# Performance work log

Measured on AMD Instinct MI355X. Metric: run time of the kernel, lower is better.

Reference implementation:

```python
import jax, jax.numpy as jnp
import numpy as np

D = 2048
H = 16
HD = 128
INNER = H * HD
EPS = 1e-6


def rmsnorm(x, w):
    var = jnp.mean(x * x, axis=-1, keepdims=True)
    return x * jax.lax.rsqrt(var + EPS) * w


def setup_inputs() -> dict:
    key = jax.random.key(0)
    ks = jax.random.split(key, 10)
    B, T, N_ws, T_corr = 2, 2048, 64, 512
    scale = 1.0 / np.sqrt(D)
    return {
        "hidden_states": jax.random.normal(ks[0], (B, T, D), jnp.float32),
        "workspace": jax.random.normal(ks[1], (B, N_ws, D), jnp.float32),
        "correction_tokens": jax.random.normal(ks[2], (B, T_corr, D), jnp.float32),
        "correction_mask": jax.random.randint(ks[3], (B, T_corr), 0, 2, jnp.int32),
        "ln_q_w": jnp.ones((D,), jnp.float32),
        "ln_kv_w": jnp.ones((D,), jnp.float32),
        "Wq": jax.random.normal(ks[4], (D, INNER), jnp.float32) * scale,
        "Wk": jax.random.normal(ks[5], (D, INNER), jnp.float32) * scale,
        "Wv": jax.random.normal(ks[6], (D, INNER), jnp.float32) * scale,
        "Wo": jax.random.normal(ks[7], (INNER, D), jnp.float32) * scale,
    }


def reference(hidden_states, workspace, correction_tokens, correction_mask,
              ln_q_w, ln_kv_w, Wq, Wk, Wv, Wo):
    B, T, _ = hidden_states.shape
    N_ws = workspace.shape[1]
    # kv context = [workspace ; correction_tokens]
    kv_context = jnp.concatenate([workspace, correction_tokens], axis=1)  # (B, N_kv, D)
    N_kv = kv_context.shape[1]
    ws_mask = jnp.ones((B, N_ws), hidden_states.dtype)
    kv_mask = jnp.concatenate([ws_mask, correction_mask.astype(hidden_states.dtype)], axis=1)  # (B, N_kv)

    h = rmsnorm(hidden_states, ln_q_w)
    kv = rmsnorm(kv_context, ln_kv_w)

    q = (h @ Wq).reshape(B, T, H, HD)        # (B,T,H,hd)
    k = (kv @ Wk).reshape(B, N_kv, H, HD)
    v = (kv @ Wv).reshape(B, N_kv, H, HD)

    scores = jnp.einsum("bthd,bshd->bhts", q, k) / np.sqrt(HD)  # (B,H,T,N_kv)
    mask = (kv_mask != 0)[:, None, None, :]                      # (B,1,1,N_kv)
    scores = jnp.where(mask, scores, -jnp.inf)
    attn = jax.nn.softmax(scores, axis=-1)
    attn = jnp.nan_to_num(attn, nan=0.0)
    # dropout is identity in eval mode
    out = jnp.einsum("bhts,bshd->bthd", attn, v).reshape(B, T, INNER)
    return out @ Wo
```

## Files before the change

kernel.cpp:

```cpp
#include <hip/hip_runtime.h>
#include <hip/hip_bf16.h>
#include <math.h>

typedef __bf16 bf16;
typedef __attribute__((ext_vector_type(8))) __bf16 bf16x8;
typedef __attribute__((ext_vector_type(4))) __bf16 bf16x4;
typedef __attribute__((ext_vector_type(4))) float f32x4;

#define D_DIM 2048
#define NKV   576

__device__ inline void gld_lds16(const void* g, void* l) {
    void* gg = const_cast<void*>(g);
    __builtin_amdgcn_global_load_lds(
        (__attribute__((address_space(1))) void*)gg,
        (__attribute__((address_space(3))) void*)l, 16, 0, 0);
}

__global__ __launch_bounds__(256) void prep(
    const float* __restrict__ hidden, const float* __restrict__ wsp,
    const float* __restrict__ corr, const float* __restrict__ lnq,
    const float* __restrict__ lnkv,
    const float* __restrict__ Wq, const float* __restrict__ Wk,
    const float* __restrict__ Wv, const float* __restrict__ Wo,
    bf16* __restrict__ hb, bf16* __restrict__ kvb,
    bf16* __restrict__ WqT, bf16* __restrict__ WkvT, bf16* __restrict__ WoT)
{
    __shared__ float tile[32][33];
    __shared__ float p[4];
    const int id = blockIdx.x, t = threadIdx.x;

    if (id < 16384) {
        const int wz = id >> 12, wy = (id >> 6) & 63, wx = id & 63;
        const float* in; bf16* out;
        switch (wz) {
            case 0:  in = Wq; out = WqT; break;
            case 1:  in = Wk; out = WkvT; break;
            case 2:  in = Wv; out = WkvT + 2048ull * 2048; break;
            default: in = Wo; out = WoT; break;
        }
        const int r0 = wy * 32, c0 = wx * 32;
        const int r = t >> 3, c = (t & 7) * 4;
        float4 v = *(const float4*)(in + (long)(r0 + r) * 2048 + c0 + c);
        tile[r][c] = v.x; tile[r][c + 1] = v.y;
        tile[r][c + 2] = v.z; tile[r][c + 3] = v.w;
        __syncthreads();
        bf16x4 o = { (bf16)tile[c][r], (bf16)tile[c + 1][r],
                     (bf16)tile[c + 2][r], (bf16)tile[c + 3][r] };
        *(bf16x4*)(out + (long)(c0 + r) * 2048 + r0 + c) = o;
        return;
    }

    const int rr0 = id - 16384;
    const float* xr; const float* w; bf16* yr;
    if (rr0 < 4096) {
        xr = hidden + (long)rr0 * D_DIM; w = lnq; yr = hb + (long)rr0 * D_DIM;
    } else if (rr0 < 4224) {
        const int rr = rr0 - 4096;
        xr = wsp + (long)rr * D_DIM; w = lnkv;
        yr = kvb + ((long)(rr >> 6) * NKV + (rr & 63)) * D_DIM;
    } else {
        const int rr = rr0 - 4224;
        xr = corr + (long)rr * D_DIM; w = lnkv;
        yr = kvb + ((long)(rr >> 9) * NKV + 64 + (rr & 511)) * D_DIM;
    }

    float4 v0 = *(const float4*)(xr + t * 4);
    float4 v1 = *(const float4*)(xr + 1024 + t * 4);
    float ss = v0.x * v0.x + v0.y * v0.y + v0.z * v0.z + v0.w * v0.w
             + v1.x * v1.x + v1.y * v1.y + v1.z * v1.z + v1.w * v1.w;
#pragma unroll
    for (int off = 32; off; off >>= 1) ss += __shfl_xor(ss, off);
    if ((t & 63) == 0) p[t >> 6] = ss;
    __syncthreads();
    const float rs = rsqrtf((p[0] + p[1] + p[2] + p[3]) * (1.0f / 2048.0f) + 1e-6f);

    float4 w0 = *(const float4*)(w + t * 4);
    float4 w1 = *(const float4*)(w + 1024 + t * 4);
    bf16x4 o0 = { (bf16)(v0.x * rs * w0.x), (bf16)(v0.y * rs * w0.y),
                  (bf16)(v0.z * rs * w0.z), (bf16)(v0.w * rs * w0.w) };
    bf16x4 o1 = { (bf16)(v1.x * rs * w1.x), (bf16)(v1.y * rs * w1.y),
                  (bf16)(v1.z * rs * w1.z), (bf16)(v1.w * rs * w1.w) };
    *(bf16x4*)(yr + t * 4) = o0;
    *(bf16x4*)(yr + 1024 + t * 4) = o1;
}

__global__ __launch_bounds__(256) void proj_all(
    const bf16* __restrict__ hb, const bf16* __restrict__ kvb,
    const bf16* __restrict__ WqT, const bf16* __restrict__ WkvT,
    bf16* __restrict__ qb, bf16* __restrict__ kb, bf16* __restrict__ vtb)
{
    __shared__ __align__(16) bf16 smem[128 * 132];
    bf16* As = smem;
    bf16* Bs = smem + 128 * 64;

    int id = blockIdx.x;
    const bf16 *A, *B; int m0, n0; bool isQ;
    if (id < 512) {
        isQ = true; A = hb; B = WqT;
        m0 = (id >> 4) * 128; n0 = (id & 15) * 128;
    } else {
        id -= 512;
        isQ = false; A = kvb; B = WkvT;
        m0 = (id >> 5) * 128; n0 = (id & 31) * 128;
    }
    const int tid = threadIdx.x, lane = tid & 63;
    const int wm = ((tid >> 6) >> 1) * 64, wn = ((tid >> 6) & 1) * 64;
    const int fr = lane & 15, fg = lane >> 4;

    f32x4 acc[4][4] = {};

    for (int k0 = 0; k0 < 2048; k0 += 64) {
#pragma unroll
        for (int p = 0; p < 4; ++p) {
            const int c = p * 256 + tid;
            const int r = c >> 3, cl = (c & 7) ^ (r & 7);
            gld_lds16(A + (long)(m0 + r) * 2048 + k0 + cl * 8, As + c * 8);
            gld_lds16(B + (long)(n0 + r) * 2048 + k0 + cl * 8, Bs + c * 8);
        }
        __syncthreads();
#pragma unroll
        for (int s = 0; s < 2; ++s) {
            const int sl = ((s << 2) + fg) ^ (fr & 7);
            bf16x8 af[4], bg[4];
#pragma unroll
            for (int i = 0; i < 4; ++i)
                af[i] = *(const bf16x8*)(As + (((wm + i * 16 + fr) << 3) + sl) * 8);
#pragma unroll
            for (int j = 0; j < 4; ++j)
                bg[j] = *(const bf16x8*)(Bs + (((wn + j * 16 + fr) << 3) + sl) * 8);
#pragma unroll
            for (int i = 0; i < 4; ++i)
#pragma unroll
                for (int j = 0; j < 4; ++j)
                    acc[i][j] = __builtin_amdgcn_mfma_f32_16x16x32_bf16(
                        af[i], bg[j], acc[i][j], 0, 0, 0);
        }
        __syncthreads();
    }

    const int er = fg * 4;
    if (isQ || n0 < 2048) {
        bf16* C = isQ ? qb : kb;
        const int ldc = 2048;
#pragma unroll
        for (int i = 0; i < 4; ++i)
#pragma unroll
            for (int j = 0; j < 4; ++j) {
                const int n = n0 + wn + j * 16 + fr;
#pragma unroll
                for (int r = 0; r < 4; ++r)
                    C[(long)(m0 + wm + i * 16 + er + r) * ldc + n] = (bf16)acc[i][j][r];
            }
        return;
    }

    const int h = (n0 - 2048) >> 7;
#pragma unroll
    for (int i = 0; i < 4; ++i)
#pragma unroll
        for (int j = 0; j < 4; ++j) {
            const int nl = wn + j * 16 + fr;
#pragma unroll
            for (int r = 0; r < 4; ++r)
                smem[nl * 132 + (wm + i * 16 + er + r)] = (bf16)acc[i][j][r];
        }
    __syncthreads();
#pragma unroll
    for (int p = 0; p < 16; ++p) {
        const int e = p * 1024 + tid * 4;
        const int d = e >> 7, mloc = e & 127;
        bf16x4 val = *(const bf16x4*)(smem + d * 132 + mloc);
        const int mm = m0 + mloc;
        const int bb = mm >= NKV;
        const int s = mm - bb * NKV;
        *(bf16x4*)(vtb + ((long)((bb * 16 + h) * 128 + d)) * NKV + s) = val;
    }
}

__global__ __launch_bounds__(256) void gemm_final(
    const bf16* __restrict__ A, const bf16* __restrict__ B, float* __restrict__ C)
{
    __shared__ __align__(16) bf16 As[128 * 64];
    __shared__ __align__(16) bf16 Bs[128 * 64];

    const int m0 = blockIdx.y * 128, n0 = blockIdx.x * 128;
    const int tid = threadIdx.x, lane = tid & 63;
    const int wm = ((tid >> 6) >> 1) * 64, wn = ((tid >> 6) & 1) * 64;
    const int fr = lane & 15, fg = lane >> 4;

    f32x4 acc[4][4] = {};

    for (int k0 = 0; k0 < 2048; k0 += 64) {
#pragma unroll
        for (int p = 0; p < 4; ++p) {
            const int c = p * 256 + tid;
            const int r = c >> 3, cl = (c & 7) ^ (r & 7);
            gld_lds16(A + (long)(m0 + r) * 2048 + k0 + cl * 8, As + c * 8);
            gld_lds16(B + (long)(n0 + r) * 2048 + k0 + cl * 8, Bs + c * 8);
        }
        __syncthreads();
#pragma unroll
        for (int s = 0; s < 2; ++s) {
            const int sl = ((s << 2) + fg) ^ (fr & 7);
            bf16x8 af[4], bg[4];
#pragma unroll
            for (int i = 0; i < 4; ++i)
                af[i] = *(const bf16x8*)(As + (((wm + i * 16 + fr) << 3) + sl) * 8);
#pragma unroll
            for (int j = 0; j < 4; ++j)
                bg[j] = *(const bf16x8*)(Bs + (((wn + j * 16 + fr) << 3) + sl) * 8);
#pragma unroll
            for (int i = 0; i < 4; ++i)
#pragma unroll
                for (int j = 0; j < 4; ++j)
                    acc[i][j] = __builtin_amdgcn_mfma_f32_16x16x32_bf16(
                        af[i], bg[j], acc[i][j], 0, 0, 0);
        }
        __syncthreads();
    }

    const int er = fg * 4;
#pragma unroll
    for (int i = 0; i < 4; ++i)
#pragma unroll
        for (int j = 0; j < 4; ++j) {
            const int n = n0 + wn + j * 16 + fr;
#pragma unroll
            for (int r = 0; r < 4; ++r)
                C[(long)(m0 + wm + i * 16 + er + r) * 2048 + n] = acc[i][j][r];
        }
}

__global__ __launch_bounds__(256, 4) void flash_attn(
    const bf16* __restrict__ Q, const bf16* __restrict__ K,
    const bf16* __restrict__ VT, const int* __restrict__ cmask,
    bf16* __restrict__ O)
{
    __shared__ __align__(16) bf16 Ks[64 * 128];
    __shared__ __align__(16) bf16 VTs[128 * 64];

    const int qt = blockIdx.x, h = blockIdx.y, b = blockIdx.z;
    const int tid = threadIdx.x, lane = tid & 63, w = tid >> 6;
    const int fr = lane & 15, fg = lane >> 4;

    const bf16* qbase = Q + ((long)(b * 2048 + qt * 64)) * 2048 + h * 128;
    bf16x8 qf[4];
#pragma unroll
    for (int s = 0; s < 4; ++s)
        qf[s] = *(const bf16x8*)(qbase + (long)(w * 16 + fr) * 2048 + s * 32 + fg * 8);

    float m_r[4], l_r[4];
    f32x4 acc_o[8];
#pragma unroll
    for (int r = 0; r < 4; ++r) { m_r[r] = -3.0e38f; l_r[r] = 0.f; }
#pragma unroll
    for (int j = 0; j < 8; ++j) acc_o[j] = (f32x4){0.f, 0.f, 0.f, 0.f};

    const float scale2 = 0.12752792330124195f;
    const bf16* kbase = K + (long)b * NKV * 2048 + h * 128;
    const bf16* vbase = VT + ((long)(b * 16 + h)) * 128 * NKV;

    for (int kc = 0; kc < 9; ++kc) {
        const int kv0 = kc * 64;
#pragma unroll
        for (int p = 0; p < 4; ++p) {
            const int c = p * 256 + tid;
            const int r = c >> 4, cs = c & 15, cl = cs ^ (r & 15);
            gld_lds16(kbase + (long)(kv0 + r) * 2048 + cl * 8, Ks + c * 8);
        }
#pragma unroll
        for (int p = 0; p < 4; ++p) {
            const int c = p * 256 + tid;
            const int r = c >> 3, cs = c & 7, cl = cs ^ (r & 7);
            gld_lds16(vbase + (long)r * NKV + kv0 + cl * 8, VTs + c * 8);
        }
        __syncthreads();

        f32x4 acc_s[4] = {};
#pragma unroll
        for (int s = 0; s < 4; ++s) {
#pragma unroll
            for (int j = 0; j < 4; ++j) {
                bf16x8 bg = *(const bf16x8*)(Ks +
                    ((j * 16 + fr) * 16 + ((s * 4 + fg) ^ fr)) * 8);
                acc_s[j] = __builtin_amdgcn_mfma_f32_16x16x32_bf16(qf[s], bg, acc_s[j], 0, 0, 0);
            }
        }

        float bias[4];
#pragma unroll
        for (int j = 0; j < 4; ++j) {
            const int kv = kv0 + j * 16 + fr;
            const bool valid = (kv < 64) || (cmask[b * 512 + kv - 64] != 0);
            bias[j] = valid ? 0.f : -1e30f;
        }
        float s_f[4][4];
        float mc[4] = {-3.0e38f, -3.0e38f, -3.0e38f, -3.0e38f};
#pragma unroll
        for (int j = 0; j < 4; ++j)
#pragma unroll
            for (int r = 0; r < 4; ++r) {
                float v = fmaf(acc_s[j][r], scale2, bias[j]);
                s_f[j][r] = v; mc[r] = fmaxf(mc[r], v);
            }
#pragma unroll
        for (int r = 0; r < 4; ++r) {
            mc[r] = fmaxf(mc[r], __shfl_xor(mc[r], 1));
            mc[r] = fmaxf(mc[r], __shfl_xor(mc[r], 2));
            mc[r] = fmaxf(mc[r], __shfl_xor(mc[r], 4));
            mc[r] = fmaxf(mc[r], __shfl_xor(mc[r], 8));
        }
        float alpha[4];
#pragma unroll
        for (int r = 0; r < 4; ++r) {
            const float mn = fmaxf(m_r[r], mc[r]);
            alpha[r] = __builtin_amdgcn_exp2f(m_r[r] - mn);
            m_r[r] = mn;
        }
        float rs[4] = {0.f, 0.f, 0.f, 0.f};
#pragma unroll
        for (int j = 0; j < 4; ++j)
#pragma unroll
            for (int r = 0; r < 4; ++r) {
                const float pv = __builtin_amdgcn_exp2f(s_f[j][r] - m_r[r]);
                s_f[j][r] = pv; rs[r] += pv;
            }
#pragma unroll
        for (int r = 0; r < 4; ++r) {
            rs[r] += __shfl_xor(rs[r], 1);
            rs[r] += __shfl_xor(rs[r], 2);
            rs[r] += __shfl_xor(rs[r], 4);
            rs[r] += __shfl_xor(rs[r], 8);
            l_r[r] = l_r[r] * alpha[r] + rs[r];
        }
#pragma unroll
        for (int j = 0; j < 8; ++j)
#pragma unroll
            for (int r = 0; r < 4; ++r) acc_o[j][r] *= alpha[r];

        __syncthreads();

        bf16* Ps = Ks;
#pragma unroll
        for (int j = 0; j < 4; ++j)
#pragma unroll
            for (int r = 0; r < 4; ++r)
                Ps[(w * 16 + fg * 4 + r) * 72 + j * 16 + fr] = (bf16)s_f[j][r];

#pragma unroll
        for (int s2 = 0; s2 < 2; ++s2) {
            bf16x8 af = *(const bf16x8*)(Ps + (w * 16 + fr) * 72 + s2 * 32 + fg * 8);
#pragma unroll
            for (int jd = 0; jd < 8; ++jd) {
                bf16x8 bg = *(const bf16x8*)(VTs +
                    ((jd * 16 + fr) * 8 + ((s2 * 4 + fg) ^ (fr & 7))) * 8);
                acc_o[jd] = __builtin_amdgcn_mfma_f32_16x16x32_bf16(af, bg, acc_o[jd], 0, 0, 0);
            }
        }
        __syncthreads();
    }

    bf16* obase = O + ((long)(b * 2048 + qt * 64)) * 2048 + h * 128;
#pragma unroll
    for (int r = 0; r < 4; ++r) {
        const float inv = 1.0f / l_r[r];
        const int row = w * 16 + fg * 4 + r;
#pragma unroll
        for (int jd = 0; jd < 8; ++jd)
            obase[(long)row * 2048 + jd * 16 + fr] = (bf16)(acc_o[jd][r] * inv);
    }
}

extern "C" void kernel_launch(void* const* d_in, const int* in_sizes, int n_in,
                              void* d_out, int out_size, void* d_ws, size_t ws_size,
                              hipStream_t stream)
{
    const float* hidden = (const float*)d_in[0];
    const float* wsp    = (const float*)d_in[1];
    const float* corr   = (const float*)d_in[2];
    const int*   cmask  = (const int*)d_in[3];
    const float* lnq    = (const float*)d_in[4];
    const float* lnkv   = (const float*)d_in[5];
    const float* Wq     = (const float*)d_in[6];
    const float* Wk     = (const float*)d_in[7];
    const float* Wv     = (const float*)d_in[8];
    const float* Wo     = (const float*)d_in[9];
    float* out = (float*)d_out;

    char* ws = (char*)d_ws;
    size_t off = 0;
    auto alloc = [&](size_t sz) { void* p = ws + off; off += (sz + 255) & ~(size_t)255; return p; };

    bf16* WqT   = (bf16*)alloc(2048ull * 2048 * 2);
    bf16* WkvT  = (bf16*)alloc(4096ull * 2048 * 2);
    bf16* WoT   = (bf16*)alloc(2048ull * 2048 * 2);
    bf16* hb    = (bf16*)alloc(4096ull * 2048 * 2);
    bf16* kvb   = (bf16*)alloc(1152ull * 2048 * 2);
    bf16* qb    = (bf16*)alloc(4096ull * 2048 * 2);
    bf16* kb    = (bf16*)alloc(1152ull * 2048 * 2);
    bf16* vtb   = (bf16*)alloc(4096ull * NKV * 2);
    bf16* aob   = (bf16*)alloc(4096ull * 2048 * 2);

    prep<<<21632, 256, 0, stream>>>(hidden, wsp, corr, lnq, lnkv,
                                    Wq, Wk, Wv, Wo, hb, kvb, WqT, WkvT, WoT);
    proj_all<<<800, 256, 0, stream>>>(hb, kvb, WqT, WkvT, qb, kb, vtb);
    flash_attn<<<dim3(32, 16, 2), 256, 0, stream>>>(qb, kb, vtb, cmask, aob);
    gemm_final<<<dim3(16, 32), 256, 0, stream>>>(aob, WoT, out);
}
```

Before: 325.0 us.

## Rewrite projection and output GEMMs as 8-wave 256-tile ping-pong pipelined kernels

Both the QKV projection and the output GEMM move from 128x128 single-buffered tiles with 4 waves to 512-thread blocks with 256-row tiles. They use double-buffered LDS (even/odd stages), async global-to-LDS loads interleaved with MFMA phases under fine-grained barriers and vmcnt waits, and s_setprio around MFMA bursts. Block IDs are remapped for L2 locality. The goal is to hide global load latency and raise arithmetic intensity, at the cost of more LDS and registers per block. The kv buffer is padded to 1280 rows so the final tile may read past the valid 1152 rows, and stores are guarded against those rows.

```diff
diff --git a/kernel.cpp b/kernel.cpp
--- a/kernel.cpp
+++ b/kernel.cpp
@@ -16,6 +16,9 @@
         (__attribute__((address_space(1))) void*)gg,
         (__attribute__((address_space(3))) void*)l, 16, 0, 0);
 }
+
+#define PH_BARRIER() do { __builtin_amdgcn_s_barrier(); asm volatile("" ::: "memory"); } while (0)
+#define VMCNT(n)     asm volatile("s_waitcnt vmcnt(" #n ")" ::: "memory")
 
 __global__ __launch_bounds__(256) void prep(
     const float* __restrict__ hidden, const float* __restrict__ wsp,
@@ -85,140 +88,251 @@
     *(bf16x4*)(yr + 1024 + t * 4) = o1;
 }
 
-__global__ __launch_bounds__(256) void proj_all(
+__global__ __launch_bounds__(512, 2) void proj_all(
     const bf16* __restrict__ hb, const bf16* __restrict__ kvb,
     const bf16* __restrict__ WqT, const bf16* __restrict__ WkvT,
     bf16* __restrict__ qb, bf16* __restrict__ kb, bf16* __restrict__ vtb)
 {
-    __shared__ __align__(16) bf16 smem[128 * 132];
-    bf16* As = smem;
-    bf16* Bs = smem + 128 * 64;
-
-    int id = blockIdx.x;
+    __shared__ __align__(16) bf16 smem[4][16384];
+    bf16* const EA = smem[0]; bf16* const EB = smem[1];
+    bf16* const OA = smem[2]; bf16* const OB = smem[3];
+
+    const int id0 = blockIdx.x;
+    const int id = (id0 & 7) * 26 + (id0 >> 3);
     const bf16 *A, *B; int m0, n0; bool isQ;
-    if (id < 512) {
-        isQ = true; A = hb; B = WqT;
-        m0 = (id >> 4) * 128; n0 = (id & 15) * 128;
+    if (id < 128) {
+        isQ = true;  A = hb;  B = WqT;
+        m0 = (id >> 3) * 256; n0 = (id & 7) * 256;
     } else {
-        id -= 512;
+        const int kd = id - 128;
         isQ = false; A = kvb; B = WkvT;
-        m0 = (id >> 5) * 128; n0 = (id & 31) * 128;
-    }
-    const int tid = threadIdx.x, lane = tid & 63;
-    const int wm = ((tid >> 6) >> 1) * 64, wn = ((tid >> 6) & 1) * 64;
+        m0 = (kd >> 4) * 256; n0 = (kd & 15) * 256;
+    }
+
+    const int tid = threadIdx.x, lane = tid & 63, w = tid >> 6;
+    const int wm = (w >> 2) * 128, wn = (w & 3) * 64;
     const int fr = lane & 15, fg = lane >> 4;
 
-    f32x4 acc[4][4] = {};
-
-    for (int k0 = 0; k0 < 2048; k0 += 64) {
-#pragma unroll
-        for (int p = 0; p < 4; ++p) {
-            const int c = p * 256 + tid;
+    f32x4 acc[8][4] = {};
+    bf16x8 af[4][2], bg[4][2];
+
+    auto stage = [&](const bf16* base, int row0, int k, bf16* dst) {
+#pragma unroll
+        for (int q = 0; q < 2; ++q) {
+            const int c = q * 512 + tid;
             const int r = c >> 3, cl = (c & 7) ^ (r & 7);
-            gld_lds16(A + (long)(m0 + r) * 2048 + k0 + cl * 8, As + c * 8);
-            gld_lds16(B + (long)(n0 + r) * 2048 + k0 + cl * 8, Bs + c * 8);
-        }
-        __syncthreads();
-#pragma unroll
-        for (int s = 0; s < 2; ++s) {
-            const int sl = ((s << 2) + fg) ^ (fr & 7);
-            bf16x8 af[4], bg[4];
+            gld_lds16(base + (long)(row0 + r) * 2048 + k + cl * 8, dst + c * 8);
+        }
+    };
+    auto load_af = [&](const bf16* t, int ib) {
+#pragma unroll
+        for (int i = 0; i < 4; ++i)
+#pragma unroll
+            for (int s = 0; s < 2; ++s) {
+                const int row = wm + (ib + i) * 16 + fr;
+                af[i][s] = *(const bf16x8*)(t + ((row << 3) + ((s * 4 + fg) ^ (fr & 7))) * 8);
+            }
+    };
+    auto load_bg = [&](const bf16* t, int jb) {
+#pragma unroll
+        for (int j = 0; j < 2; ++j)
+#pragma unroll
+            for (int s = 0; s < 2; ++s) {
+                const int row = wn + (jb + j) * 16 + fr;
+                bg[jb + j][s] = *(const bf16x8*)(t + ((row << 3) + ((s * 4 + fg) ^ (fr & 7))) * 8);
+            }
+    };
+    auto mfma16 = [&](int ib, int jb) {
+        __builtin_amdgcn_s_setprio(1);
+#pragma unroll
+        for (int s = 0; s < 2; ++s)
 #pragma unroll
             for (int i = 0; i < 4; ++i)
-                af[i] = *(const bf16x8*)(As + (((wm + i * 16 + fr) << 3) + sl) * 8);
-#pragma unroll
-            for (int j = 0; j < 4; ++j)
-                bg[j] = *(const bf16x8*)(Bs + (((wn + j * 16 + fr) << 3) + sl) * 8);
-#pragma unroll
-            for (int i = 0; i < 4; ++i)
-#pragma unroll
-                for (int j = 0; j < 4; ++j)
-                    acc[i][j] = __builtin_amdgcn_mfma_f32_16x16x32_bf16(
-                        af[i], bg[j], acc[i][j], 0, 0, 0);
-        }
-        __syncthreads();
-    }
+#pragma unroll
+                for (int j = 0; j < 2; ++j)
+                    acc[ib + i][jb + j] = __builtin_amdgcn_mfma_f32_16x16x32_bf16(
+                        af[i][s], bg[jb + j][s], acc[ib + i][jb + j], 0, 0, 0);
+        __builtin_amdgcn_s_setprio(0);
+    };
+
+    stage(A, m0,        0, EA); stage(A, m0 + 128,  0, EA + 8192);
+    stage(B, n0,        0, EB); stage(B, n0 + 128,  0, EB + 8192);
+    stage(B, n0,       64, OB); stage(B, n0 + 128, 64, OB + 8192);
+    VMCNT(4);
+    PH_BARRIER();
+
+    for (int it = 0; it < 16; ++it) {
+        const int kO  = (it * 128 +  64) & 2047;
+        const int kE2 = (it * 128 + 128) & 2047;
+        const int kO2 = (it * 128 + 192) & 2047;
+        load_af(EA, 0); load_bg(EB, 0);
+        stage(A, m0, kO, OA);
+        PH_BARRIER(); mfma16(0, 0); PH_BARRIER();
+        load_bg(EB, 2);
+        stage(A, m0 + 128, kO, OA + 8192);
+        PH_BARRIER(); mfma16(0, 2); PH_BARRIER();
+        load_af(EA, 4);
+        stage(B, n0, kE2, EB);
+        PH_BARRIER(); mfma16(4, 2); PH_BARRIER();
+        stage(B, n0 + 128, kE2, EB + 8192);
+        PH_BARRIER(); mfma16(4, 0); VMCNT(4); PH_BARRIER();
+        load_af(OA, 0); load_bg(OB, 0);
+        stage(A, m0, kE2, EA);
+        PH_BARRIER(); mfma16(0, 0); PH_BARRIER();
+        load_bg(OB, 2);
+        stage(A, m0 + 128, kE2, EA + 8192);
+        PH_BARRIER(); mfma16(0, 2); PH_BARRIER();
+        load_af(OA, 4);
+        stage(B, n0, kO2, OB);
+        PH_BARRIER(); mfma16(4, 2); PH_BARRIER();
+        stage(B, n0 + 128, kO2, OB + 8192);
+        PH_BARRIER(); mfma16(4, 0); VMCNT(4); PH_BARRIER();
+    }
+
+    VMCNT(0);
+    __syncthreads();
 
     const int er = fg * 4;
     if (isQ || n0 < 2048) {
         bf16* C = isQ ? qb : kb;
-        const int ldc = 2048;
-#pragma unroll
-        for (int i = 0; i < 4; ++i)
+        const int mlim = isQ ? 4096 : 1152;
+#pragma unroll
+        for (int i = 0; i < 8; ++i)
 #pragma unroll
             for (int j = 0; j < 4; ++j) {
                 const int n = n0 + wn + j * 16 + fr;
 #pragma unroll
-                for (int r = 0; r < 4; ++r)
-                    C[(long)(m0 + wm + i * 16 + er + r) * ldc + n] = (bf16)acc[i][j][r];
+                for (int r = 0; r < 4; ++r) {
+                    const int m = m0 + wm + i * 16 + er + r;
+                    if (m < mlim)
+                        C[(long)m * 2048 + n] = (bf16)acc[i][j][r];
+                }
             }
         return;
     }
 
-    const int h = (n0 - 2048) >> 7;
-#pragma unroll
-    for (int i = 0; i < 4; ++i)
-#pragma unroll
-        for (int j = 0; j < 4; ++j) {
-            const int nl = wn + j * 16 + fr;
-#pragma unroll
-            for (int r = 0; r < 4; ++r)
-                smem[nl * 132 + (wm + i * 16 + er + r)] = (bf16)acc[i][j][r];
-        }
+    bf16* T = &smem[0][0];
+#pragma unroll
+    for (int p = 0; p < 2; ++p) {
+        if (p) __syncthreads();
+        if ((wn >> 7) == p) {
+            const int nb = wn - p * 128;
+#pragma unroll
+            for (int i = 0; i < 8; ++i)
+#pragma unroll
+                for (int j = 0; j < 4; ++j) {
+                    const int nl = nb + j * 16 + fr;
+#pragma unroll
+                    for (int r = 0; r < 4; ++r)
+                        T[nl * 264 + wm + i * 16 + er + r] = (bf16)acc[i][j][r];
+                }
+        }
+        __syncthreads();
+        const int hh = (n0 - 2048 + p * 128) >> 7;
+        for (int e = tid; e < 128 * 64; e += 512) {
+            const int d = e >> 6, mg = (e & 63) * 4;
+            const int mm = m0 + mg;
+            if (mm < 1152) {
+                bf16x4 val = *(const bf16x4*)(T + d * 264 + mg);
+                const int bb = mm >= NKV;
+                const int s = mm - bb * NKV;
+                *(bf16x4*)(vtb + ((long)((bb * 16 + hh) * 128 + d)) * NKV + s) = val;
+            }
+        }
+    }
+}
+
+__global__ __launch_bounds__(512, 2) void gemm_final(
+    const bf16* __restrict__ Ag, const bf16* __restrict__ Bg, float* __restrict__ C)
+{
+    __shared__ __align__(16) bf16 smem[49152];
+    bf16* const EA = smem;           bf16* const EB = smem + 16384;
+    bf16* const OA = smem + 24576;   bf16* const OB = smem + 40960;
+
+    const int id0 = blockIdx.x;
+    const int id = (id0 & 7) * 32 + (id0 >> 3);
+    const int m0 = (id >> 4) * 256, n0 = (id & 15) * 128;
+
+    const int tid = threadIdx.x, lane = tid & 63, w = tid >> 6;
+    const int wm = (w >> 1) * 64, wn = (w & 1) * 64;
+    const int fr = lane & 15, fg = lane >> 4;
+
+    f32x4 acc[4][4] = {};
+    bf16x8 af[2][2], bg[4][2];
+
+    auto stage = [&](const bf16* base, int row0, int k, bf16* dst) {
+#pragma unroll
+        for (int q = 0; q < 2; ++q) {
+            const int c = q * 512 + tid;
+            const int r = c >> 3, cl = (c & 7) ^ (r & 7);
+            gld_lds16(base + (long)(row0 + r) * 2048 + k + cl * 8, dst + c * 8);
+        }
+    };
+    auto load_af = [&](const bf16* t, int ib) {
+#pragma unroll
+        for (int i = 0; i < 2; ++i)
+#pragma unroll
+            for (int s = 0; s < 2; ++s) {
+                const int row = wm + (ib + i) * 16 + fr;
+                af[i][s] = *(const bf16x8*)(t + ((row << 3) + ((s * 4 + fg) ^ (fr & 7))) * 8);
+            }
+    };
+    auto load_bg = [&](const bf16* t, int jb) {
+#pragma unroll
+        for (int j = 0; j < 2; ++j)
+#pragma unroll
+            for (int s = 0; s < 2; ++s) {
+                const int row = wn + (jb + j) * 16 + fr;
+                bg[jb + j][s] = *(const bf16x8*)(t + ((row << 3) + ((s * 4 + fg) ^ (fr & 7))) * 8);
+            }
+    };
+    auto mfma8 = [&](int ib, int jb) {
+        __builtin_amdgcn_s_setprio(1);
+#pragma unroll
+        for (int s = 0; s < 2; ++s)
+#pragma unroll
+            for (int i = 0; i < 2; ++i)
+#pragma unroll
+                for (int j = 0; j < 2; ++j)
+                    acc[ib + i][jb + j] = __builtin_amdgcn_mfma_f32_16x16x32_bf16(
+                        af[i][s], bg[jb + j][s], acc[ib + i][jb + j], 0, 0, 0);
+        __builtin_amdgcn_s_setprio(0);
+    };
+
+    stage(Ag, m0,       0, EA); stage(Ag, m0 + 128, 0, EA + 8192);
+    stage(Bg, n0,       0, EB);
+    stage(Bg, n0,      64, OB);
+    VMCNT(2);
+    PH_BARRIER();
+
+    for (int it = 0; it < 16; ++it) {
+        const int kO  = (it * 128 +  64) & 2047;
+        const int kE2 = (it * 128 + 128) & 2047;
+        const int kO2 = (it * 128 + 192) & 2047;
+        load_af(EA, 0); load_bg(EB, 0);
+        stage(Ag, m0, kO, OA);
+        PH_BARRIER(); mfma8(0, 0); PH_BARRIER();
+        load_bg(EB, 2);
+        stage(Ag, m0 + 128, kO, OA + 8192);
+        PH_BARRIER(); mfma8(0, 2); PH_BARRIER();
+        load_af(EA, 2);
+        stage(Bg, n0, kE2, EB);
+        PH_BARRIER(); mfma8(2, 2); PH_BARRIER();
+        stage(Ag, m0, kE2, EA);
+        PH_BARRIER(); mfma8(2, 0); VMCNT(4); PH_BARRIER();
+        load_af(OA, 0); load_bg(OB, 0);
+        stage(Ag, m0 + 128, kE2, EA + 8192);
+        PH_BARRIER(); mfma8(0, 0); PH_BARRIER();
+        load_bg(OB, 2);
+        PH_BARRIER(); mfma8(0, 2); PH_BARRIER();
+        load_af(OA, 2);
+        stage(Bg, n0, kO2, OB);
+        PH_BARRIER(); mfma8(2, 2); PH_BARRIER();
+        PH_BARRIER(); mfma8(2, 0); VMCNT(2); PH_BARRIER();
+    }
+
+    VMCNT(0);
     __syncthreads();
-#pragma unroll
-    for (int p = 0; p < 16; ++p) {
-        const int e = p * 1024 + tid * 4;
-        const int d = e >> 7, mloc = e & 127;
-        bf16x4 val = *(const bf16x4*)(smem + d * 132 + mloc);
-        const int mm = m0 + mloc;
-        const int bb = mm >= NKV;
-        const int s = mm - bb * NKV;
-        *(bf16x4*)(vtb + ((long)((bb * 16 + h) * 128 + d)) * NKV + s) = val;
-    }
-}
-
-__global__ __launch_bounds__(256) void gemm_final(
-    const bf16* __restrict__ A, const bf16* __restrict__ B, float* __restrict__ C)
-{
-    __shared__ __align__(16) bf16 As[128 * 64];
-    __shared__ __align__(16) bf16 Bs[128 * 64];
-
-    const int m0 = blockIdx.y * 128, n0 = blockIdx.x * 128;
-    const int tid = threadIdx.x, lane = tid & 63;
-    const int wm = ((tid >> 6) >> 1) * 64, wn = ((tid >> 6) & 1) * 64;
-    const int fr = lane & 15, fg = lane >> 4;
-
-    f32x4 acc[4][4] = {};
-
-    for (int k0 = 0; k0 < 2048; k0 += 64) {
-#pragma unroll
-        for (int p = 0; p < 4; ++p) {
-            const int c = p * 256 + tid;
-            const int r = c >> 3, cl = (c & 7) ^ (r & 7);
-            gld_lds16(A + (long)(m0 + r) * 2048 + k0 + cl * 8, As + c * 8);
-            gld_lds16(B + (long)(n0 + r) * 2048 + k0 + cl * 8, Bs + c * 8);
-        }
-        __syncthreads();
-#pragma unroll
-        for (int s = 0; s < 2; ++s) {
-            const int sl = ((s << 2) + fg) ^ (fr & 7);
-            bf16x8 af[4], bg[4];
-#pragma unroll
-            for (int i = 0; i < 4; ++i)
-                af[i] = *(const bf16x8*)(As + (((wm + i * 16 + fr) << 3) + sl) * 8);
-#pragma unroll
-            for (int j = 0; j < 4; ++j)
-                bg[j] = *(const bf16x8*)(Bs + (((wn + j * 16 + fr) << 3) + sl) * 8);
-#pragma unroll
-            for (int i = 0; i < 4; ++i)
-#pragma unroll
-                for (int j = 0; j < 4; ++j)
-                    acc[i][j] = __builtin_amdgcn_mfma_f32_16x16x32_bf16(
-                        af[i], bg[j], acc[i][j], 0, 0, 0);
-        }
-        __syncthreads();
-    }
 
     const int er = fg * 4;
 #pragma unroll
@@ -396,7 +510,7 @@
     bf16* WkvT  = (bf16*)alloc(4096ull * 2048 * 2);
     bf16* WoT   = (bf16*)alloc(2048ull * 2048 * 2);
     bf16* hb    = (bf16*)alloc(4096ull * 2048 * 2);
-    bf16* kvb   = (bf16*)alloc(1152ull * 2048 * 2);
+    bf16* kvb   = (bf16*)alloc(1280ull * 2048 * 2);
     bf16* qb    = (bf16*)alloc(4096ull * 2048 * 2);
     bf16* kb    = (bf16*)alloc(1152ull * 2048 * 2);
     bf16* vtb   = (bf16*)alloc(4096ull * NKV * 2);
@@ -404,7 +518,7 @@
 
     prep<<<21632, 256, 0, stream>>>(hidden, wsp, corr, lnq, lnkv,
                                     Wq, Wk, Wv, Wo, hb, kvb, WqT, WkvT, WoT);
-    proj_all<<<800, 256, 0, stream>>>(hb, kvb, WqT, WkvT, qb, kb, vtb);
+    proj_all<<<208, 512, 0, stream>>>(hb, kvb, WqT, WkvT, qb, kb, vtb);
     flash_attn<<<dim3(32, 16, 2), 256, 0, stream>>>(qb, kb, vtb, cmask, aob);
-    gemm_final<<<dim3(16, 32), 256, 0, stream>>>(aob, WoT, out);
+    gemm_final<<<256, 512, 0, stream>>>(aob, WoT, out);
 }
```

Measured after the change: 297.7 us. -8.4%, faster.
